# Kernel optimization log

Hardware: AMD Instinct MI355X
Metric: run time of the kernel (lower is better)

Reference implementation:

```python
import jax, jax.numpy as jnp
import numpy as np

N_NODES = 50000
N_EDGES = 640000
DIM_IN = 128
DIM_OUT = 32
HEADS = 4
NEG_SLOPE = 0.2


def setup_inputs() -> dict:
    key = jax.random.key(0)
    ks = jax.random.split(key, 8)
    HC = HEADS * DIM_OUT
    x = jax.random.normal(ks[0], (N_NODES, DIM_IN), dtype=jnp.float32)
    edge_index = jax.random.randint(ks[1], (2, N_EDGES), 0, N_NODES, dtype=jnp.int32)
    s = 1.0 / np.sqrt(DIM_IN)
    Wl = jax.random.normal(ks[2], (DIM_IN, HC), dtype=jnp.float32) * s   # lin_l (source)
    Wr = jax.random.normal(ks[3], (DIM_IN, HC), dtype=jnp.float32) * s   # lin_r (target)
    att = jax.random.normal(ks[4], (HEADS, DIM_OUT), dtype=jnp.float32) * (1.0 / np.sqrt(DIM_OUT))
    bias = jnp.zeros((HC,), dtype=jnp.float32)
    Wp = jax.random.normal(ks[5], (HC, DIM_OUT), dtype=jnp.float32) * (1.0 / np.sqrt(HC))
    bp = jnp.zeros((DIM_OUT,), dtype=jnp.float32)
    return {"x": x, "edge_index": edge_index, "Wl": Wl, "Wr": Wr,
            "att": att, "bias": bias, "Wp": Wp, "bp": bp}


def reference(x, edge_index, Wl, Wr, att, bias, Wp, bp):
    N = x.shape[0]
    H, C = att.shape
    src = edge_index[0]  # j: message source
    dst = edge_index[1]  # i: message target (softmax segment)
    xl = (x @ Wl).reshape(N, H, C)  # source-side transform
    xr = (x @ Wr).reshape(N, H, C)  # target-side transform
    # GATv2: e_ij = a^T LeakyReLU(xl_j + xr_i)
    e = jax.nn.leaky_relu(xl[src] + xr[dst], NEG_SLOPE)        # [E,H,C]
    logits = jnp.einsum('ehc,hc->eh', e, att)                  # [E,H]
    m = jax.ops.segment_max(logits, dst, num_segments=N)       # [N,H]
    ex = jnp.exp(logits - m[dst])
    denom = jax.ops.segment_sum(ex, dst, num_segments=N)       # [N,H]
    alpha = ex / (denom[dst] + 1e-16)                          # [E,H]
    msg = xl[src] * alpha[:, :, None]                          # [E,H,C]
    out = jax.ops.segment_sum(msg, dst, num_segments=N)        # [N,H,C]
    out = out.reshape(N, H * C) + bias                         # concat heads + bias
    return out @ Wp + bp                                       # proj to dim_out
```

## Files before the change

### kernel.cpp

```cpp
#include <hip/hip_runtime.h>
#include <hip/hip_bf16.h>
#include <math.h>

#define N_NODES 50000
#define N_EDGES 640000
#define HEADS 4
#define CDIM 32
#define HC 128
#define DIN 128
#define DOUT 32
#define NEG_SLOPE 0.2f
#define TPAD 136
#define BCAP 64
#define NPB 16
#define EPT 4
#define ZERO_NB ((N_NODES + 255) / 256)
#define WT_NB (2 * DIN * HC / 256)
#define WPT_NB (DOUT * HC / 256)
#define FILL_NB (N_EDGES / (256 * EPT))
#define TF_NB ((N_NODES + 127) / 128)

typedef __hip_bfloat16 bf16;
typedef __attribute__((ext_vector_type(8))) short short8;
typedef __attribute__((ext_vector_type(4))) float floatx4;
typedef __attribute__((ext_vector_type(4))) unsigned short ushort4v;

static __device__ __forceinline__ float bflo(unsigned w) { return __uint_as_float(w << 16); }
static __device__ __forceinline__ float bfhi(unsigned w) { return __uint_as_float(w & 0xFFFF0000u); }
static __device__ __forceinline__ unsigned short f2bf(float f) {
    union { bf16 h; unsigned short u; } cv; cv.h = __float2bfloat16(f); return cv.u;
}

__global__ __launch_bounds__(256) void k_prep(
    unsigned* __restrict__ cnt,
    const float* __restrict__ Wl, const float* __restrict__ Wr,
    const float* __restrict__ bias, const float* __restrict__ Wp,
    const float* __restrict__ bp,
    bf16* __restrict__ WlF, bf16* __restrict__ WrF, bf16* __restrict__ WpT,
    float* __restrict__ cvec)
{
    const int t = threadIdx.x, b = blockIdx.x;
    if (b < ZERO_NB) {
        const int i = b * 256 + t;
        if (i < N_NODES) cnt[i] = 0u;
    } else if (b < ZERO_NB + WT_NB) {
        const int i = (b - ZERO_NB) * 256 + t;
        const int i2 = (i < DIN * HC) ? i : i - DIN * HC;
        const int c = i2 >> 7, j = i2 & 127;
        const int jt = j >> 4, m = j & 15;
        const int kk = c >> 5, quad = (c >> 3) & 3, u = c & 7;
        const int idx = (jt * 4 + kk) * 512 + (quad * 16 + m) * 8 + u;
        if (i < DIN * HC) WlF[idx] = __float2bfloat16(Wl[i2]);
        else              WrF[idx] = __float2bfloat16(Wr[i2]);
    } else if (b < ZERO_NB + WT_NB + WPT_NB) {
        const int i = (b - ZERO_NB - WT_NB) * 256 + t;
        const int c = i >> 5, j = i & 31;
        WpT[j * HC + c] = __float2bfloat16(Wp[i]);
    } else if (t < DOUT) {
        float v = bp[t];
        for (int c = 0; c < HC; c++) v += bias[c] * Wp[c * DOUT + t];
        cvec[t] = v;
    }
}

__global__ __launch_bounds__(256) void k_fill(
    const int* __restrict__ ei, unsigned* __restrict__ cnt,
    int* __restrict__ srcs)
{
    const int e0 = (blockIdx.x * 256 + threadIdx.x) * EPT;
    const int4 sv = *(const int4*)(ei + e0);
    const int4 dv = *(const int4*)(ei + N_EDGES + e0);
    const int s[4] = {sv.x, sv.y, sv.z, sv.w};
    const int d[4] = {dv.x, dv.y, dv.z, dv.w};
    unsigned pos[4];
    #pragma unroll
    for (int i = 0; i < EPT; i++)
        pos[i] = atomicAdd(&cnt[d[i]], 1u);
    #pragma unroll
    for (int i = 0; i < EPT; i++)
        if (pos[i] < BCAP) srcs[((size_t)d[i] << 6) + pos[i]] = s[i];
}

__global__ __launch_bounds__(256) void k_tf(
    const float* __restrict__ x,
    const bf16* __restrict__ WlF, const bf16* __restrict__ WrF,
    bf16* __restrict__ xl, bf16* __restrict__ xr)
{
    const int t = threadIdx.x, b = blockIdx.x;
    const int n0 = b * 128;
    const int w = t >> 6, lane = t & 63;
    const int m = lane & 15, quad = lane >> 4;
    const int na = n0 + w * 32 + m;
    const int nb = na + 16;
    const bool va = (na < N_NODES), vb = (nb < N_NODES);

    const float* xpa = x + (size_t)(va ? na : 0) * DIN;
    const float* xpb = x + (size_t)(vb ? nb : 0) * DIN;
    short8 afa[4], afb[4];
    #pragma unroll
    for (int kk = 0; kk < 4; kk++) {
        const float4 la = *(const float4*)(xpa + kk * 32 + quad * 8);
        const float4 ha = *(const float4*)(xpa + kk * 32 + quad * 8 + 4);
        const float4 lb = *(const float4*)(xpb + kk * 32 + quad * 8);
        const float4 hb = *(const float4*)(xpb + kk * 32 + quad * 8 + 4);
        short8 va8, vb8;
        va8[0] = (short)f2bf(la.x); va8[1] = (short)f2bf(la.y);
        va8[2] = (short)f2bf(la.z); va8[3] = (short)f2bf(la.w);
        va8[4] = (short)f2bf(ha.x); va8[5] = (short)f2bf(ha.y);
        va8[6] = (short)f2bf(ha.z); va8[7] = (short)f2bf(ha.w);
        vb8[0] = (short)f2bf(lb.x); vb8[1] = (short)f2bf(lb.y);
        vb8[2] = (short)f2bf(lb.z); vb8[3] = (short)f2bf(lb.w);
        vb8[4] = (short)f2bf(hb.x); vb8[5] = (short)f2bf(hb.y);
        vb8[6] = (short)f2bf(hb.z); vb8[7] = (short)f2bf(hb.w);
        afa[kk] = va8;
        afb[kk] = vb8;
    }

    const short8* wlf = (const short8*)WlF;
    const short8* wrf = (const short8*)WrF;
    #pragma unroll
    for (int jt = 0; jt < 8; jt++) {
        floatx4 aLa = {0.f,0.f,0.f,0.f}, aLb = {0.f,0.f,0.f,0.f};
        floatx4 aRa = {0.f,0.f,0.f,0.f}, aRb = {0.f,0.f,0.f,0.f};
        #pragma unroll
        for (int kk = 0; kk < 4; kk++) {
            const short8 bl = wlf[(jt * 4 + kk) * 64 + lane];
            const short8 br = wrf[(jt * 4 + kk) * 64 + lane];
            aLa = __builtin_amdgcn_mfma_f32_16x16x32_bf16(bl, afa[kk], aLa, 0, 0, 0);
            aLb = __builtin_amdgcn_mfma_f32_16x16x32_bf16(bl, afb[kk], aLb, 0, 0, 0);
            aRa = __builtin_amdgcn_mfma_f32_16x16x32_bf16(br, afa[kk], aRa, 0, 0, 0);
            aRb = __builtin_amdgcn_mfma_f32_16x16x32_bf16(br, afb[kk], aRb, 0, 0, 0);
        }
        const int joff = jt * 16 + quad * 4;
        if (va) {
            ushort4v pl, pr;
            #pragma unroll
            for (int r = 0; r < 4; r++) { pl[r] = f2bf(aLa[r]); pr[r] = f2bf(aRa[r]); }
            *(ushort4v*)(xl + (size_t)na * HC + joff) = pl;
            *(ushort4v*)(xr + (size_t)na * HC + joff) = pr;
        }
        if (vb) {
            ushort4v pl, pr;
            #pragma unroll
            for (int r = 0; r < 4; r++) { pl[r] = f2bf(aLb[r]); pr[r] = f2bf(aRb[r]); }
            *(ushort4v*)(xl + (size_t)nb * HC + joff) = pl;
            *(ushort4v*)(xr + (size_t)nb * HC + joff) = pr;
        }
    }
}

static __device__ __forceinline__ uint4 gat(
    const int srcj, const int e, const int cn,
    const unsigned* __restrict__ xl2, const int hq)
{
    const int s = __shfl(srcj, e & 63, 64);
    const size_t row = (size_t)((e < cn) ? s : 0) << 6;
    return ((const uint4*)(xl2 + row))[hq];
}

static __device__ __forceinline__ void consume_edge(
    const uint4 bx, const int eidx, const int cn,
    const float* __restrict__ xr_, const float* __restrict__ a_,
    float& s_run, float* __restrict__ acc)
{
    float x_[8];
    x_[0] = bflo(bx.x); x_[1] = bfhi(bx.x);
    x_[2] = bflo(bx.y); x_[3] = bfhi(bx.y);
    x_[4] = bflo(bx.z); x_[5] = bfhi(bx.z);
    x_[6] = bflo(bx.w); x_[7] = bfhi(bx.w);
    float p = 0.f;
    #pragma unroll
    for (int k = 0; k < 8; k++) {
        float v = x_[k] + xr_[k];
        v = fmaxf(v, NEG_SLOPE * v);
        p = fmaf(a_[k], v, p);
    }
    p += __shfl_xor(p, 1, 64);
    p += __shfl_xor(p, 2, 64);
    const float e_ = (eidx < cn) ? __expf(p) : 0.f;
    s_run += e_;
    #pragma unroll
    for (int k = 0; k < 8; k++) acc[k] = fmaf(x_[k], e_, acc[k]);
}

__global__ __launch_bounds__(256) void k_agg(
    const int* __restrict__ srcs, const unsigned* __restrict__ cnt,
    const unsigned* __restrict__ xl2,
    const unsigned* __restrict__ xr2,
    const float* __restrict__ att,
    const bf16* __restrict__ WpT,
    const float* __restrict__ cvec,
    float* __restrict__ out)
{
    __shared__ __align__(16) unsigned short srow[NPB][TPAD];
    const int t = threadIdx.x;
    const int w = t >> 6, lane = t & 63;
    const int es = lane >> 4, hq = lane & 15;

    const float4 av0 = ((const float4*)att)[hq * 2];
    const float4 av1 = ((const float4*)att)[hq * 2 + 1];
    const float a_[8] = {av0.x, av0.y, av0.z, av0.w, av1.x, av1.y, av1.z, av1.w};

    const int nb0 = blockIdx.x * NPB + w * 4;
    const uint4 cv4 = *(const uint4*)(cnt + nb0);
    int cns[4];
    cns[0] = (int)(cv4.x < 64u ? cv4.x : 64u);
    cns[1] = (int)(cv4.y < 64u ? cv4.y : 64u);
    cns[2] = (int)(cv4.z < 64u ? cv4.z : 64u);
    cns[3] = (int)(cv4.w < 64u ? cv4.w : 64u);
    int srcjv[4];
    uint4 xru[4];
    #pragma unroll
    for (int ni = 0; ni < 4; ni++) {
        srcjv[ni] = srcs[((size_t)(nb0 + ni) << 6) + lane];
        xru[ni] = ((const uint4*)(xr2 + (size_t)(nb0 + ni) * 64))[hq];
    }

    #pragma unroll
    for (int ni = 0; ni < 4; ni++) {
        const int cn = cns[ni];
        float xr_[8];
        xr_[0] = bflo(xru[ni].x); xr_[1] = bfhi(xru[ni].x);
        xr_[2] = bflo(xru[ni].y); xr_[3] = bfhi(xru[ni].y);
        xr_[4] = bflo(xru[ni].z); xr_[5] = bfhi(xru[ni].z);
        xr_[6] = bflo(xru[ni].w); xr_[7] = bfhi(xru[ni].w);
        float s_run = 0.f;
        float acc[8] = {0.f, 0.f, 0.f, 0.f, 0.f, 0.f, 0.f, 0.f};
        const int sj = srcjv[ni];

        uint4 b0 = gat(sj, es,      cn, xl2, hq);
        uint4 b1 = gat(sj, es + 4,  cn, xl2, hq);
        uint4 b2 = gat(sj, es + 8,  cn, xl2, hq);
        uint4 b3 = gat(sj, es + 12, cn, xl2, hq);
        for (int i = 0; i < cn; i += 16) {
            const bool more = (i + 16 < cn);
            consume_edge(b0, i + es,      cn, xr_, a_, s_run, acc);
            if (more) b0 = gat(sj, i + 16 + es, cn, xl2, hq);
            consume_edge(b1, i + es + 4,  cn, xr_, a_, s_run, acc);
            if (more) b1 = gat(sj, i + 20 + es, cn, xl2, hq);
            consume_edge(b2, i + es + 8,  cn, xr_, a_, s_run, acc);
            if (more) b2 = gat(sj, i + 24 + es, cn, xl2, hq);
            consume_edge(b3, i + es + 12, cn, xr_, a_, s_run, acc);
            if (more) b3 = gat(sj, i + 28 + es, cn, xl2, hq);
        }
        s_run += __shfl_xor(s_run, 16, 64);
        s_run += __shfl_xor(s_run, 32, 64);
        #pragma unroll
        for (int k = 0; k < 8; k++) {
            acc[k] += __shfl_xor(acc[k], 16, 64);
            acc[k] += __shfl_xor(acc[k], 32, 64);
        }
        const float rden = 1.f / (s_run + 1e-16f);

        if (es == 0) {
            union { unsigned short s[8]; uint4 v; } pk;
            #pragma unroll
            for (int k = 0; k < 8; k++) pk.s[k] = f2bf(acc[k] * rden);
            *(uint4*)&srow[w * 4 + ni][hq * 8] = pk.v;
        }
    }
    __syncthreads();

    if (w < 2) {
        const int m = lane & 15, quad = lane >> 4;
        short8 af[4];
        #pragma unroll
        for (int kk = 0; kk < 4; kk++)
            af[kk] = *(const short8*)&srow[m][kk * 32 + quad * 8];
        floatx4 d = {0.f, 0.f, 0.f, 0.f};
        #pragma unroll
        for (int kk = 0; kk < 4; kk++) {
            const short8 bfr = *(const short8*)(WpT + (w * 16 + m) * HC + kk * 32 + quad * 8);
            d = __builtin_amdgcn_mfma_f32_16x16x32_bf16(af[kk], bfr, d, 0, 0, 0);
        }
        const int jj = w * 16 + m;
        const float cv = cvec[jj];
        #pragma unroll
        for (int r = 0; r < 4; r++) {
            const int node = blockIdx.x * NPB + quad * 4 + r;
            out[(size_t)node * DOUT + jj] = d[r] + cv;
        }
    }
}

extern "C" void kernel_launch(void* const* d_in, const int* in_sizes, int n_in,
                              void* d_out, int out_size, void* d_ws, size_t ws_size,
                              hipStream_t stream)
{
    const float* x    = (const float*)d_in[0];
    const int*   ei   = (const int*)d_in[1];
    const float* Wl   = (const float*)d_in[2];
    const float* Wr   = (const float*)d_in[3];
    const float* att  = (const float*)d_in[4];
    const float* bias = (const float*)d_in[5];
    const float* Wp   = (const float*)d_in[6];
    const float* bp   = (const float*)d_in[7];
    float* out = (float*)d_out;

    bf16* xl       = (bf16*)d_ws;
    bf16* xr       = xl + (size_t)N_NODES * HC;
    bf16* WlF      = xr + (size_t)N_NODES * HC;
    bf16* WrF      = WlF + DIN * HC;
    bf16* WpT      = WrF + DIN * HC;
    float* cvec    = (float*)(WpT + DOUT * HC);
    unsigned* cnt  = (unsigned*)(cvec + DOUT);
    int* srcs      = (int*)(cnt + N_NODES);

    k_prep<<<ZERO_NB + WT_NB + WPT_NB + 1, 256, 0, stream>>>(
        cnt, Wl, Wr, bias, Wp, bp, WlF, WrF, WpT, cvec);
    k_fill<<<FILL_NB, 256, 0, stream>>>(ei, cnt, srcs);
    k_tf<<<TF_NB, 256, 0, stream>>>(x, WlF, WrF, xl, xr);
    k_agg<<<N_NODES / NPB, 256, 0, stream>>>(srcs, cnt,
        (const unsigned*)xl, (const unsigned*)xr, att, WpT, cvec, out);
}
```

Before: 171.5 us.

## Fuse edge-fill and transform kernels, store source ids as 16-bit

The edge bucketing kernel and the node-transform GEMM kernel are merged into one launch that dispatches on block index, so the two independent stages can run concurrently and one launch gap disappears. The per-destination source list is stored as unsigned short instead of int, which halves the scattered writes in fill and the reads in aggregation. This relies on node ids staying below 65536. The bias/projection constant vector is now reduced in parallel across 256 threads through shared memory instead of by 32 threads looping serially.

```diff
diff --git a/kernel.cpp b/kernel.cpp
--- a/kernel.cpp
+++ b/kernel.cpp
@@ -56,38 +56,50 @@
         const int i = (b - ZERO_NB - WT_NB) * 256 + t;
         const int c = i >> 5, j = i & 31;
         WpT[j * HC + c] = __float2bfloat16(Wp[i]);
-    } else if (t < DOUT) {
-        float v = bp[t];
-        for (int c = 0; c < HC; c++) v += bias[c] * Wp[c * DOUT + t];
-        cvec[t] = v;
-    }
-}
-
-__global__ __launch_bounds__(256) void k_fill(
+    } else {
+        __shared__ float part[8][32];
+        const int j = t & 31, ch = t >> 5;
+        float v = 0.f;
+        for (int c = ch * 16; c < ch * 16 + 16; c++)
+            v += bias[c] * Wp[c * DOUT + j];
+        part[ch][j] = v;
+        __syncthreads();
+        if (t < 32) {
+            float s = bp[t];
+            #pragma unroll
+            for (int k = 0; k < 8; k++) s += part[k][t];
+            cvec[t] = s;
+        }
+    }
+}
+
+__global__ __launch_bounds__(256) void k_fill_tf(
     const int* __restrict__ ei, unsigned* __restrict__ cnt,
-    int* __restrict__ srcs)
-{
-    const int e0 = (blockIdx.x * 256 + threadIdx.x) * EPT;
-    const int4 sv = *(const int4*)(ei + e0);
-    const int4 dv = *(const int4*)(ei + N_EDGES + e0);
-    const int s[4] = {sv.x, sv.y, sv.z, sv.w};
-    const int d[4] = {dv.x, dv.y, dv.z, dv.w};
-    unsigned pos[4];
-    #pragma unroll
-    for (int i = 0; i < EPT; i++)
-        pos[i] = atomicAdd(&cnt[d[i]], 1u);
-    #pragma unroll
-    for (int i = 0; i < EPT; i++)
-        if (pos[i] < BCAP) srcs[((size_t)d[i] << 6) + pos[i]] = s[i];
-}
-
-__global__ __launch_bounds__(256) void k_tf(
+    unsigned short* __restrict__ srcs,
     const float* __restrict__ x,
     const bf16* __restrict__ WlF, const bf16* __restrict__ WrF,
     bf16* __restrict__ xl, bf16* __restrict__ xr)
 {
     const int t = threadIdx.x, b = blockIdx.x;
-    const int n0 = b * 128;
+
+    if (b < FILL_NB) {
+        const int e0 = (b * 256 + t) * EPT;
+        const int4 sv = *(const int4*)(ei + e0);
+        const int4 dv = *(const int4*)(ei + N_EDGES + e0);
+        const int s[4] = {sv.x, sv.y, sv.z, sv.w};
+        const int d[4] = {dv.x, dv.y, dv.z, dv.w};
+        unsigned pos[4];
+        #pragma unroll
+        for (int i = 0; i < EPT; i++)
+            pos[i] = atomicAdd(&cnt[d[i]], 1u);
+        #pragma unroll
+        for (int i = 0; i < EPT; i++)
+            if (pos[i] < BCAP)
+                srcs[((size_t)d[i] << 6) + pos[i]] = (unsigned short)s[i];
+        return;
+    }
+
+    const int n0 = (b - FILL_NB) * 128;
     const int w = t >> 6, lane = t & 63;
     const int m = lane & 15, quad = lane >> 4;
     const int na = n0 + w * 32 + m;
@@ -184,7 +196,7 @@
 }
 
 __global__ __launch_bounds__(256) void k_agg(
-    const int* __restrict__ srcs, const unsigned* __restrict__ cnt,
+    const unsigned short* __restrict__ srcs, const unsigned* __restrict__ cnt,
     const unsigned* __restrict__ xl2,
     const unsigned* __restrict__ xr2,
     const float* __restrict__ att,
@@ -212,7 +224,7 @@
     uint4 xru[4];
     #pragma unroll
     for (int ni = 0; ni < 4; ni++) {
-        srcjv[ni] = srcs[((size_t)(nb0 + ni) << 6) + lane];
+        srcjv[ni] = (int)srcs[((size_t)(nb0 + ni) << 6) + lane];
         xru[ni] = ((const uint4*)(xr2 + (size_t)(nb0 + ni) * 64))[hq];
     }
 
@@ -304,12 +316,12 @@
     bf16* WpT      = WrF + DIN * HC;
     float* cvec    = (float*)(WpT + DOUT * HC);
     unsigned* cnt  = (unsigned*)(cvec + DOUT);
-    int* srcs      = (int*)(cnt + N_NODES);
+    unsigned short* srcs = (unsigned short*)(cnt + N_NODES);
 
     k_prep<<<ZERO_NB + WT_NB + WPT_NB + 1, 256, 0, stream>>>(
         cnt, Wl, Wr, bias, Wp, bp, WlF, WrF, WpT, cvec);
-    k_fill<<<FILL_NB, 256, 0, stream>>>(ei, cnt, srcs);
-    k_tf<<<TF_NB, 256, 0, stream>>>(x, WlF, WrF, xl, xr);
+    k_fill_tf<<<FILL_NB + TF_NB, 256, 0, stream>>>(ei, cnt, srcs, x,
+                                                   WlF, WrF, xl, xr);
     k_agg<<<N_NODES / NPB, 256, 0, stream>>>(srcs, cnt,
         (const unsigned*)xl, (const unsigned*)xr, att, WpT, cvec, out);
 }
```

Measured after the change: 169.7 us. Within noise of the previous version (-1.0%).
